# Optimization experiments

Measured on AMD Instinct MI355X. Metric: run time of the kernel, lower is better.

## Reference

```python
import jax, jax.numpy as jnp
import numpy as np

D, H, L, NB = 128, 8, 2, 32
NEIGHBOR_DIST = 50.0
OUT_H, PRED = 512, 60
N, A, T = 32, 50, 50
DH = D // H
FF = 4 * D


def setup_inputs():
    key = jax.random.key(0)
    ks = jax.random.split(key, 20)
    g = lambda k, s, sc=0.02: jax.random.normal(k, s, jnp.float32) * sc
    return {
        "x": jax.random.normal(ks[0], (N, A, T, 5), jnp.float32) * 10.0,
        "invalid_entries": jax.random.randint(ks[1], (N, A, T), 0, 2).astype(bool),
        "emb_W": g(ks[2], (5, D)), "emb_b": jnp.zeros((D,), jnp.float32),
        "dist_emb": g(ks[3], (NB, H)),
        "ln_g": jnp.ones((L, 3, D), jnp.float32), "ln_b": jnp.zeros((L, 3, D), jnp.float32),
        "Wq": g(ks[4], (L, 2, D, D)), "Wk": g(ks[5], (L, 2, D, D)),
        "Wv": g(ks[6], (L, 2, D, D)), "Wo": g(ks[7], (L, 2, D, D)),
        "ffn_W1": g(ks[8], (L, D, FF)), "ffn_b1": jnp.zeros((L, FF), jnp.float32),
        "ffn_W2": g(ks[9], (L, FF, D)), "ffn_b2": jnp.zeros((L, D), jnp.float32),
        "mlp_W1": g(ks[10], (D, OUT_H)), "mlp_b1": jnp.zeros((OUT_H,), jnp.float32),
        "mlp_W2": g(ks[11], (OUT_H, 2 * PRED)), "mlp_b2": jnp.zeros((2 * PRED,), jnp.float32),
    }


def _ln(h, g, b):
    mu = h.mean(-1, keepdims=True)
    var = ((h - mu) ** 2).mean(-1, keepdims=True)
    return (h - mu) / jnp.sqrt(var + 1e-5) * g + b


def _mha(h, Wq, Wk, Wv, Wo, mask, bias=None):
    # h: (B, S, D); mask: (B, S, S) bool, True = blocked; bias: (B, H, S, S)
    B, S, _ = h.shape
    q = (h @ Wq).reshape(B, S, H, DH)
    k = (h @ Wk).reshape(B, S, H, DH)
    v = (h @ Wv).reshape(B, S, H, DH)
    s = jnp.einsum('bqhd,bkhd->bhqk', q, k) / jnp.sqrt(jnp.float32(DH))
    if bias is not None:
        s = s + bias
    s = jnp.where(mask[:, None, :, :], jnp.float32(-1e9), s)
    a = jax.nn.softmax(s, axis=-1)
    o = jnp.einsum('bhqk,bkhd->bqhd', a, v).reshape(B, S, D)
    return o @ Wo


def _masks_and_bias(x, invalid_entries, dist_emb):
    # pos: (N*T, A, 2); masks are non-differentiable, stop grad through cdist
    pos = jax.lax.stop_gradient(jnp.swapaxes(x, 1, 2).reshape(N * T, A, 5)[:, :, :2])
    dist = jnp.sqrt(jnp.sum((pos[:, :, None, :] - pos[:, None, :, :]) ** 2, axis=-1))
    bin_size = NEIGHBOR_DIST / NB
    bucket = jnp.clip((dist / bin_size).astype(jnp.int32), 0, NB - 1)
    dist_bias = jnp.transpose(dist_emb[bucket], (0, 3, 1, 2))  # (N*T, H, A, A)

    inv_s = jnp.swapaxes(invalid_entries, 1, 2).reshape(N * T, A)
    ego_only = jnp.ones((A, A), bool).at[0, :].set(False)  # only ego row attends broadly
    social = (dist > NEIGHBOR_DIST) | inv_s[:, None, :] | ego_only[None]
    di_a = jnp.arange(min(50, A))
    social = social.at[:, di_a, di_a].set(False)  # vectorized form of the 50-iter loop

    inv_t = invalid_entries.reshape(N * A, T)
    temporal = jnp.triu(jnp.ones((T, T), bool), 1)[None] | inv_t[:, None, :]
    di_t = jnp.arange(min(50, T))
    temporal = temporal.at[:, di_t, di_t].set(False)
    return temporal, social, dist_bias


def _forward(x, invalid_entries, emb_W, emb_b, dist_emb, ln_g, ln_b,
             Wq, Wk, Wv, Wo, ffn_W1, ffn_b1, ffn_W2, ffn_b2,
             mlp_W1, mlp_b1, mlp_W2, mlp_b2):
    temporal_mask, social_mask, dist_bias = _masks_and_bias(x, invalid_entries, dist_emb)
    h = x @ emb_W + emb_b  # (N, A, T, D)
    for l in range(L):
        # temporal attention over T per agent
        ht = h.reshape(N * A, T, D)
        ht = ht + _mha(_ln(ht, ln_g[l, 0], ln_b[l, 0]),
                       Wq[l, 0], Wk[l, 0], Wv[l, 0], Wo[l, 0], temporal_mask)
        h = ht.reshape(N, A, T, D)
        # social attention over A per timestep, with bucketized distance bias
        hs = jnp.swapaxes(h, 1, 2).reshape(N * T, A, D)
        hs = hs + _mha(_ln(hs, ln_g[l, 1], ln_b[l, 1]),
                       Wq[l, 1], Wk[l, 1], Wv[l, 1], Wo[l, 1], social_mask, bias=dist_bias)
        h = jnp.swapaxes(hs.reshape(N, T, A, D), 1, 2)
        # FFN
        hn = _ln(h, ln_g[l, 2], ln_b[l, 2])
        h = h + (jnp.maximum(hn @ ffn_W1[l] + ffn_b1[l], 0.0) @ ffn_W2[l] + ffn_b2[l])
    e = h[:, 0]  # ego agent: (N, T, D)
    e = (e @ mlp_W1 + mlp_b1) @ mlp_W2 + mlp_b2  # two linears, no activation (as in source)
    return e.reshape(N, T, PRED, 2)


def reference(x, invalid_entries, emb_W, emb_b, dist_emb, ln_g, ln_b,
              Wq, Wk, Wv, Wo, ffn_W1, ffn_b1, ffn_W2, ffn_b2,
              mlp_W1, mlp_b1, mlp_W2, mlp_b2):
    return _forward(x, invalid_entries, emb_W, emb_b, dist_emb, ln_g, ln_b,
                    Wq, Wk, Wv, Wo, ffn_W1, ffn_b1, ffn_W2, ffn_b2,
                    mlp_W1, mlp_b1, mlp_W2, mlp_b2)
```

## Files before the change

### kernel.cpp

```cpp
#include <hip/hip_runtime.h>


#define DD 128
typedef __attribute__((ext_vector_type(8))) short bf16x8;
typedef __attribute__((ext_vector_type(4))) float f32x4;
#define MFMA16(a, b, c) __builtin_amdgcn_mfma_f32_16x16x32_bf16(a, b, c, 0, 0, 0)

__device__ __forceinline__ float bf2f(unsigned short u) {
  union { unsigned int i; float f; } x; x.i = ((unsigned int)u) << 16; return x.f;
}
__device__ __forceinline__ unsigned short f2bf(float f) {
  union { float f; unsigned int i; } x; x.f = f;
  return (unsigned short)((x.i + 0x7FFFu + ((x.i >> 16) & 1u)) >> 16);
}
__device__ __forceinline__ float wave_sum(float v) {
#pragma unroll
  for (int off = 32; off > 0; off >>= 1) v += __shfl_xor(v, off, 64);
  return v;
}
__device__ __forceinline__ float wave_max(float v) {
#pragma unroll
  for (int off = 32; off > 0; off >>= 1) v = fmaxf(v, __shfl_xor(v, off, 64));
  return v;
}
__device__ __forceinline__ bool load_inv(const void* p, int idx, int bytemode) {
  if (bytemode) return ((const unsigned char*)p)[idx] != 0;
  return ((const int*)p)[idx] != 0;
}

__global__ void detect_kernel(const void* __restrict__ inv, int* __restrict__ flag) {
  __shared__ int found;
  if (threadIdx.x == 0) found = 0;
  __syncthreads();
  const unsigned char* p = (const unsigned char*)inv;
  int loc = 0;
  for (int i = threadIdx.x; i < 16384; i += blockDim.x)
    if ((i & 3) != 0 && p[i] != 0) loc = 1;
  if (loc) atomicOr(&found, 1);
  __syncthreads();
  if (threadIdx.x == 0) *flag = found ? 1 : 0;
}

__global__ __launch_bounds__(256) void convert_weights(
    const float* __restrict__ Wq, const float* __restrict__ Wk,
    const float* __restrict__ Wv, const float* __restrict__ Wo,
    const float* __restrict__ W1, const float* __restrict__ W2,
    const float* __restrict__ W1m, const float* __restrict__ W2m,
    unsigned short* __restrict__ wqkv, unsigned short* __restrict__ wot,
    unsigned short* __restrict__ w1t, unsigned short* __restrict__ w2t,
    unsigned short* __restrict__ w1e, unsigned short* __restrict__ w2e) {
  __shared__ float tile[32][33];
  int b = blockIdx.x;
  int tx = threadIdx.x & 31, ty = threadIdx.x >> 5;
  const float* src; unsigned short* dst;
  int o0, i0, srcld, dstld, osub = 0, obound = 1 << 30;
  if (b < 192) {
    int m = b / 48, t2 = b % 48;
    o0 = (t2 / 4) * 32; i0 = (t2 % 4) * 32;
    int sel = o0 >> 7;
    src = (sel == 0 ? Wq : (sel == 1 ? Wk : Wv)) + m * 16384;
    osub = sel * 128; srcld = 128;
    dst = wqkv + m * 49152; dstld = 128;
  } else if (b < 256) {
    int m = (b - 192) / 16, t2 = (b - 192) % 16;
    o0 = (t2 / 4) * 32; i0 = (t2 % 4) * 32;
    src = Wo + m * 16384; srcld = 128;
    dst = wot + m * 16384; dstld = 128;
  } else if (b < 384) {
    int l = (b - 256) / 64, t2 = (b - 256) % 64;
    o0 = (t2 / 4) * 32; i0 = (t2 % 4) * 32;
    src = W1 + l * 65536; srcld = 512;
    dst = w1t + l * 65536; dstld = 128;
  } else if (b < 512) {
    int l = (b - 384) / 64, t2 = (b - 384) % 64;
    o0 = (t2 / 16) * 32; i0 = (t2 % 16) * 32;
    src = W2 + l * 65536; srcld = 128;
    dst = w2t + l * 65536; dstld = 512;
  } else if (b < 576) {
    int t2 = b - 512;
    o0 = (t2 / 4) * 32; i0 = (t2 % 4) * 32;
    src = W1m; srcld = 512;
    dst = w1e; dstld = 128;
  } else {
    int t2 = b - 576;
    o0 = (t2 / 16) * 32; i0 = (t2 % 16) * 32;
    src = W2m; srcld = 120; obound = 120;
    dst = w2e; dstld = 512;
  }
#pragma unroll
  for (int kk = 0; kk < 4; ++kk) {
    int i = i0 + ty + 8 * kk, o = o0 + tx;
    tile[ty + 8 * kk][tx] = (o < obound) ? src[i * srcld + (o - osub)] : 0.f;
  }
  __syncthreads();
#pragma unroll
  for (int kk = 0; kk < 4; ++kk) {
    int o = o0 + ty + 8 * kk, i = i0 + tx;
    dst[o * dstld + i] = f2bf(tile[tx][ty + 8 * kk]);
  }
}

__global__ __launch_bounds__(512, 4) void temporal_attn_kernel(
    const float* __restrict__ x, float* __restrict__ h,
    const void* __restrict__ inv, const int* __restrict__ flagp,
    const float* __restrict__ g, const float* __restrict__ bb,
    const float* __restrict__ embW, const float* __restrict__ embB,
    const unsigned short* __restrict__ wqkv,
    const unsigned short* __restrict__ wot, int first) {
  __shared__ __align__(16) unsigned short xbf[64][136];
  __shared__ __align__(16) unsigned short kbf[64][136];
  __shared__ __align__(16) unsigned short vT[128][72];
  __shared__ __align__(16) unsigned short pbuf[8][16][72];
  __shared__ float ssb[8][64];
  int seq = blockIdx.x;
  int tid = threadIdx.x, lane = tid & 63, wid = tid >> 6;
  unsigned long long invmask =
      __ballot((lane < 50) && load_inv(inv, seq * 50 + lane, *flagp));
  const f32x4 zf = (f32x4){0.f, 0.f, 0.f, 0.f};
  if (first) {
    for (int t = wid; t < 50; t += 8) {
      int tok = seq * 50 + t;
      float c0 = x[tok * 5], c1 = x[tok * 5 + 1], c2 = x[tok * 5 + 2];
      float c3 = x[tok * 5 + 3], c4 = x[tok * 5 + 4];
      float x0 = embB[lane] + c0 * embW[lane] + c1 * embW[128 + lane] +
                 c2 * embW[256 + lane] + c3 * embW[384 + lane] + c4 * embW[512 + lane];
      float x1 = embB[lane + 64] + c0 * embW[lane + 64] + c1 * embW[128 + lane + 64] +
                 c2 * embW[256 + lane + 64] + c3 * embW[384 + lane + 64] +
                 c4 * embW[512 + lane + 64];
      h[tok * DD + lane] = x0; h[tok * DD + lane + 64] = x1;
      float mu = wave_sum(x0 + x1) * (1.0f / 128.0f);
      float d0 = x0 - mu, d1 = x1 - mu;
      float var = wave_sum(d0 * d0 + d1 * d1) * (1.0f / 128.0f);
      float rstd = rsqrtf(var + 1e-5f);
      xbf[t][lane]      = f2bf(d0 * rstd * g[lane] + bb[lane]);
      xbf[t][lane + 64] = f2bf(d1 * rstd * g[lane + 64] + bb[lane + 64]);
    }
  } else {
    float v0[7], v1[7];
#pragma unroll
    for (int i = 0; i < 7; ++i) {
      int t = wid + 8 * i;
      if (t < 50) {
        v0[i] = h[(seq * 50 + t) * DD + lane];
        v1[i] = h[(seq * 50 + t) * DD + lane + 64];
      }
    }
#pragma unroll
    for (int i = 0; i < 7; ++i) {
      int t = wid + 8 * i;
      if (t < 50) {
        float mu = wave_sum(v0[i] + v1[i]) * (1.0f / 128.0f);
        float d0 = v0[i] - mu, d1 = v1[i] - mu;
        float var = wave_sum(d0 * d0 + d1 * d1) * (1.0f / 128.0f);
        float rstd = rsqrtf(var + 1e-5f);
        xbf[t][lane]      = f2bf(d0 * rstd * g[lane] + bb[lane]);
        xbf[t][lane + 64] = f2bf(d1 * rstd * g[lane + 64] + bb[lane + 64]);
      }
    }
  }
  for (int idx = tid; idx < 1904; idx += 512) {
    int r = idx / 136, cc = idx - r * 136;
    xbf[50 + r][cc] = 0;
    kbf[50 + r][cc] = 0;
  }
  for (int idx = tid; idx < 896; idx += 512) {
    int row = idx / 7, dwi = idx - row * 7;
    ((unsigned int*)&vT[row][50])[dwi] = 0u;
  }
  __syncthreads();
  int lrow = lane & 15, lk = (lane >> 4) * 8, lr4 = (lane >> 4) * 4;
  int colb = wid * 16 + lrow;
  {
    f32x4 ac[4];
#pragma unroll
    for (int mt = 0; mt < 4; ++mt) ac[mt] = zf;
    bf16x8 wk[4];
#pragma unroll
    for (int kt = 0; kt < 4; ++kt)
      wk[kt] = *(const bf16x8*)&wqkv[((8 + wid) * 16 + lrow) * 128 + kt * 32 + lk];
#pragma unroll
    for (int kt = 0; kt < 4; ++kt)
#pragma unroll
      for (int mt = 0; mt < 4; ++mt) {
        bf16x8 a = *(const bf16x8*)&xbf[mt * 16 + lrow][kt * 32 + lk];
        ac[mt] = MFMA16(a, wk[kt], ac[mt]);
      }
#pragma unroll
    for (int mt = 0; mt < 4; ++mt)
#pragma unroll
      for (int r = 0; r < 4; ++r) {
        int row = mt * 16 + lr4 + r;
        if (row < 50) kbf[row][colb] = f2bf(ac[mt][r]);
      }
  }
  {
    f32x4 ac[4];
#pragma unroll
    for (int mt = 0; mt < 4; ++mt) ac[mt] = zf;
    bf16x8 wv[4];
#pragma unroll
    for (int kt = 0; kt < 4; ++kt)
      wv[kt] = *(const bf16x8*)&wqkv[((16 + wid) * 16 + lrow) * 128 + kt * 32 + lk];
#pragma unroll
    for (int kt = 0; kt < 4; ++kt)
#pragma unroll
      for (int mt = 0; mt < 4; ++mt) {
        bf16x8 a = *(const bf16x8*)&xbf[mt * 16 + lrow][kt * 32 + lk];
        ac[mt] = MFMA16(a, wv[kt], ac[mt]);
      }
#pragma unroll
    for (int mt = 0; mt < 4; ++mt)
#pragma unroll
      for (int r = 0; r < 4; ++r) {
        int row = mt * 16 + lr4 + r;
        if (row < 50) vT[colb][row] = f2bf(ac[mt][r]);
      }
  }
  {
    f32x4 acQ[4];
#pragma unroll
    for (int mt = 0; mt < 4; ++mt) acQ[mt] = zf;
    bf16x8 wq[4];
#pragma unroll
    for (int kt = 0; kt < 4; ++kt)
      wq[kt] = *(const bf16x8*)&wqkv[(wid * 16 + lrow) * 128 + kt * 32 + lk];
#pragma unroll
    for (int kt = 0; kt < 4; ++kt)
#pragma unroll
      for (int mt = 0; mt < 4; ++mt) {
        bf16x8 a = *(const bf16x8*)&xbf[mt * 16 + lrow][kt * 32 + lk];
        acQ[mt] = MFMA16(a, wq[kt], acQ[mt]);
      }
    __syncthreads();
#pragma unroll
    for (int mt = 0; mt < 4; ++mt)
#pragma unroll
      for (int r = 0; r < 4; ++r) {
        int row = mt * 16 + lr4 + r;
        if (row < 50) xbf[row][colb] = f2bf(acQ[mt][r] * 0.25f);
      }
  }
  __syncthreads();
  {
    int hh = wid, c = lane & 15, gq = lane >> 4;
    const int hb = hh * 16;
    bf16x8 vfr0 = *(const bf16x8*)&vT[hb + c][gq * 8];
    bf16x8 vfr1 = *(const bf16x8*)&vT[hb + c][32 + gq * 8];
#pragma unroll
    for (int nt2 = 0; nt2 < 4; ++nt2) {
      bf16x8 qf = (bf16x8){0, 0, 0, 0, 0, 0, 0, 0};
      if (gq < 2) qf = *(const bf16x8*)&xbf[nt2 * 16 + c][hb + gq * 8];
      f32x4 Cs[4];
#pragma unroll
      for (int mt = 0; mt < 4; ++mt) {
        bf16x8 kf = (bf16x8){0, 0, 0, 0, 0, 0, 0, 0};
        if (gq < 2) kf = *(const bf16x8*)&kbf[mt * 16 + c][hb + gq * 8];
        Cs[mt] = MFMA16(kf, qf, zf);
      }
      int tq = nt2 * 16 + c;
      float ss = 0.f;
#pragma unroll
      for (int mt = 0; mt < 4; ++mt) {
        float pv[4];
#pragma unroll
        for (int r = 0; r < 4; ++r) {
          int tk = mt * 16 + gq * 4 + r;
          bool ok = (tk == tq) || ((tk < tq) && !((invmask >> tk) & 1ull));
          float p = ok ? __expf(Cs[mt][r]) : 0.f;
          ss += p;
          pv[r] = p;
        }
        unsigned int* dst = (unsigned int*)&pbuf[hh][c][mt * 16 + gq * 4];
        dst[0] = (unsigned)f2bf(pv[0]) | ((unsigned)f2bf(pv[1]) << 16);
        dst[1] = (unsigned)f2bf(pv[2]) | ((unsigned)f2bf(pv[3]) << 16);
      }
      ss += __shfl_xor(ss, 16, 64);
      ss += __shfl_xor(ss, 32, 64);
      if (gq == 0) ssb[hh][tq] = 1.f / ss;
      asm volatile("s_waitcnt lgkmcnt(0)" ::: "memory");
      __builtin_amdgcn_sched_barrier(0);
      bf16x8 pf0 = *(const bf16x8*)&pbuf[hh][c][gq * 8];
      bf16x8 pf1 = *(const bf16x8*)&pbuf[hh][c][32 + gq * 8];
      f32x4 acO = MFMA16(pf0, vfr0, zf);
      acO = MFMA16(pf1, vfr1, acO);
#pragma unroll
      for (int r = 0; r < 4; ++r) {
        int tqo = nt2 * 16 + gq * 4 + r;
        if (tqo < 50) {
          float rs = ssb[hh][tqo];
          xbf[tqo][hb + c] = f2bf(acO[r] * rs);
        }
      }
    }
  }
  __syncthreads();
  {
    f32x4 acc2[4];
#pragma unroll
    for (int mt = 0; mt < 4; ++mt) acc2[mt] = zf;
    bf16x8 wo4[4];
#pragma unroll
    for (int kt = 0; kt < 4; ++kt)
      wo4[kt] = *(const bf16x8*)&wot[(wid * 16 + lrow) * 128 + kt * 32 + lk];
#pragma unroll
    for (int kt = 0; kt < 4; ++kt)
#pragma unroll
      for (int mt = 0; mt < 4; ++mt) {
        bf16x8 a = *(const bf16x8*)&xbf[mt * 16 + lrow][kt * 32 + lk];
        acc2[mt] = MFMA16(a, wo4[kt], acc2[mt]);
      }
#pragma unroll
    for (int mt = 0; mt < 4; ++mt)
#pragma unroll
      for (int r = 0; r < 4; ++r) {
        int row = mt * 16 + lr4 + r;
        if (row < 50) h[(seq * 50 + row) * DD + colb] += acc2[mt][r];
      }
  }
}

__global__ __launch_bounds__(512, 6) void social_attn_kernel(
    const float* __restrict__ x, float* __restrict__ h,
    const void* __restrict__ inv, const int* __restrict__ flagp,
    const float* __restrict__ dist_emb,
    const float* __restrict__ g, const float* __restrict__ bb,
    const unsigned short* __restrict__ wqkv,
    const unsigned short* __restrict__ wot, int ego_only) {
  __shared__ __align__(16) unsigned short xbf[64][136];
  __shared__ __align__(16) unsigned short vsb[64][136];
  __shared__ float q0s[128];
  __shared__ float aw[8][52];
  int nt_ = blockIdx.x;
  int n = nt_ / 50, t = nt_ - n * 50;
  int tid = threadIdx.x, lane = tid & 63, wid = tid >> 6;
  const f32x4 zf = (f32x4){0.f, 0.f, 0.f, 0.f};
  {
    float v0[7], v1[7];
#pragma unroll
    for (int i = 0; i < 7; ++i) {
      int j = wid + 8 * i;
      if (j < 50) {
        int tok = (n * 50 + j) * 50 + t;
        v0[i] = h[tok * DD + lane];
        v1[i] = h[tok * DD + lane + 64];
      }
    }
#pragma unroll
    for (int i = 0; i < 7; ++i) {
      int j = wid + 8 * i;
      if (j < 50) {
        float mu = wave_sum(v0[i] + v1[i]) * (1.0f / 128.0f);
        float d0 = v0[i] - mu, d1 = v1[i] - mu;
        float var = wave_sum(d0 * d0 + d1 * d1) * (1.0f / 128.0f);
        float rstd = rsqrtf(var + 1e-5f);
        xbf[j][lane]      = f2bf(d0 * rstd * g[lane] + bb[lane]);
        xbf[j][lane + 64] = f2bf(d1 * rstd * g[lane + 64] + bb[lane + 64]);
      }
    }
  }
  __syncthreads();
  int lrow = lane & 15, lk = (lane >> 4) * 8, lr4 = (lane >> 4) * 4;
  int colb = wid * 16 + lrow;
  {
    f32x4 ac[4];
#pragma unroll
    for (int mt = 0; mt < 4; ++mt) ac[mt] = zf;
    bf16x8 wv[4];
#pragma unroll
    for (int kt = 0; kt < 4; ++kt)
      wv[kt] = *(const bf16x8*)&wqkv[((16 + wid) * 16 + lrow) * 128 + kt * 32 + lk];
#pragma unroll
    for (int kt = 0; kt < 4; ++kt)
#pragma unroll
      for (int mt = 0; mt < 4; ++mt) {
        bf16x8 a = *(const bf16x8*)&xbf[mt * 16 + lrow][kt * 32 + lk];
        ac[mt] = MFMA16(a, wv[kt], ac[mt]);
      }
#pragma unroll
    for (int mt = 0; mt < 4; ++mt)
#pragma unroll
      for (int r = 0; r < 4; ++r) {
        int row = mt * 16 + lr4 + r;
        if (row < 50) vsb[row][colb] = f2bf(ac[mt][r]);
      }
  }
  {
    f32x4 acq = zf;
    bf16x8 wq[4];
#pragma unroll
    for (int kt = 0; kt < 4; ++kt)
      wq[kt] = *(const bf16x8*)&wqkv[(wid * 16 + lrow) * 128 + kt * 32 + lk];
#pragma unroll
    for (int kt = 0; kt < 4; ++kt) {
      bf16x8 a0 = *(const bf16x8*)&xbf[lrow][kt * 32 + lk];
      acq = MFMA16(a0, wq[kt], acq);
    }
    if (lane < 16) q0s[wid * 16 + lane] = acq[0];
  }
  {
    f32x4 ac[4];
#pragma unroll
    for (int mt = 0; mt < 4; ++mt) ac[mt] = zf;
    bf16x8 wk[4];
#pragma unroll
    for (int kt = 0; kt < 4; ++kt)
      wk[kt] = *(const bf16x8*)&wqkv[((8 + wid) * 16 + lrow) * 128 + kt * 32 + lk];
#pragma unroll
    for (int kt = 0; kt < 4; ++kt)
#pragma unroll
      for (int mt = 0; mt < 4; ++mt) {
        bf16x8 a = *(const bf16x8*)&xbf[mt * 16 + lrow][kt * 32 + lk];
        ac[mt] = MFMA16(a, wk[kt], ac[mt]);
      }
    __syncthreads();
#pragma unroll
    for (int mt = 0; mt < 4; ++mt)
#pragma unroll
      for (int r = 0; r < 4; ++r) {
        int row = mt * 16 + lr4 + r;
        if (row < 50) xbf[row][colb] = f2bf(ac[mt][r]);
      }
  }
  __syncthreads();
  {
    int hh = wid, j = lane;
    float s = -1e30f;
    if (j < 50) {
      float x0 = x[(n * 2500 + t) * 5 + 0];
      float y0 = x[(n * 2500 + t) * 5 + 1];
      int tokj = (n * 50 + j) * 50 + t;
      float xj = x[tokj * 5 + 0], yj = x[tokj * 5 + 1];
      float dx = x0 - xj, dy = y0 - yj;
      float dist = sqrtf(dx * dx + dy * dy);
      int bucket = (int)(dist / 1.5625f);
      bucket = bucket < 0 ? 0 : (bucket > 31 ? 31 : bucket);
      bool mk = (j != 0) && ((dist > 50.0f) || load_inv(inv, tokj, *flagp));
      bf16x8 k0 = *(const bf16x8*)&xbf[j][hh * 16];
      bf16x8 k1 = *(const bf16x8*)&xbf[j][hh * 16 + 8];
      float acc2 = 0.f;
#pragma unroll
      for (int u = 0; u < 8; ++u)
        acc2 += q0s[hh * 16 + u] * bf2f((unsigned short)k0[u]) +
                q0s[hh * 16 + 8 + u] * bf2f((unsigned short)k1[u]);
      s = mk ? -1e9f : acc2 * 0.25f + dist_emb[bucket * 8 + hh];
    }
    float m = wave_max(s);
    float p = (j < 50) ? __expf(s - m) : 0.f;
    float sm = wave_sum(p);
    if (j < 50) aw[hh][j] = p / sm;
  }
  __syncthreads();
  float a0val = 0.f;
  if (tid < 128) {
    int hh2 = tid >> 4;
#pragma unroll 10
    for (int j = 0; j < 50; ++j) a0val += aw[hh2][j] * bf2f(vsb[j][tid]);
  }
  __syncthreads();
  if (tid < 128) vsb[0][tid] = f2bf(a0val);
  __syncthreads();
  if (!ego_only) {
    f32x4 acc2[4];
#pragma unroll
    for (int mt = 0; mt < 4; ++mt) acc2[mt] = zf;
    bf16x8 wo4[4];
#pragma unroll
    for (int kt = 0; kt < 4; ++kt)
      wo4[kt] = *(const bf16x8*)&wot[(wid * 16 + lrow) * 128 + kt * 32 + lk];
#pragma unroll
    for (int kt = 0; kt < 4; ++kt)
#pragma unroll
      for (int mt = 0; mt < 4; ++mt) {
        bf16x8 a = *(const bf16x8*)&vsb[mt * 16 + lrow][kt * 32 + lk];
        acc2[mt] = MFMA16(a, wo4[kt], acc2[mt]);
      }
#pragma unroll
    for (int mt = 0; mt < 4; ++mt)
#pragma unroll
      for (int r = 0; r < 4; ++r) {
        int row = mt * 16 + lr4 + r;
        if (row < 50)
          h[((n * 50 + row) * 50 + t) * DD + colb] += acc2[mt][r];
      }
  } else {
    f32x4 acc2 = zf;
    bf16x8 wo4[4];
#pragma unroll
    for (int kt = 0; kt < 4; ++kt)
      wo4[kt] = *(const bf16x8*)&wot[(wid * 16 + lrow) * 128 + kt * 32 + lk];
#pragma unroll
    for (int kt = 0; kt < 4; ++kt) {
      bf16x8 a = *(const bf16x8*)&vsb[lrow][kt * 32 + lk];
      acc2 = MFMA16(a, wo4[kt], acc2);
    }
    if ((lane >> 4) == 0)
      h[(n * 2500 + t) * DD + colb] += acc2[0];
  }
}

__global__ __launch_bounds__(512, 6) void ffn_kernel(
    float* __restrict__ h, const float* __restrict__ g, const float* __restrict__ bb,
    const unsigned short* __restrict__ w1t, const float* __restrict__ b1,
    const unsigned short* __restrict__ w2t, const float* __restrict__ b2) {
  __shared__ __align__(16) unsigned short xbf[32][136];
  __shared__ __align__(16) unsigned short hid[32][520];
  int base = blockIdx.x * 32;
  int tid = threadIdx.x, lane = tid & 63, wid = tid >> 6;
  {
    float v0[4], v1[4];
#pragma unroll
    for (int i = 0; i < 4; ++i) {
      int tok = base + wid + 8 * i;
      v0[i] = h[tok * DD + lane];
      v1[i] = h[tok * DD + lane + 64];
    }
#pragma unroll
    for (int i = 0; i < 4; ++i) {
      int r = wid + 8 * i;
      float mu = wave_sum(v0[i] + v1[i]) * (1.0f / 128.0f);
      float d0 = v0[i] - mu, d1 = v1[i] - mu;
      float var = wave_sum(d0 * d0 + d1 * d1) * (1.0f / 128.0f);
      float rstd = rsqrtf(var + 1e-5f);
      xbf[r][lane]      = f2bf(d0 * rstd * g[lane] + bb[lane]);
      xbf[r][lane + 64] = f2bf(d1 * rstd * g[lane + 64] + bb[lane + 64]);
    }
  }
  __syncthreads();
  int lrow = lane & 15, lk = (lane >> 4) * 8, lr4 = (lane >> 4) * 4;
  {
    f32x4 acc[2][4];
#pragma unroll
    for (int mt = 0; mt < 2; ++mt)
#pragma unroll
      for (int nt = 0; nt < 4; ++nt) acc[mt][nt] = (f32x4){0.f, 0.f, 0.f, 0.f};
    bf16x8 w[2][4];
#pragma unroll
    for (int nt = 0; nt < 4; ++nt)
      w[0][nt] = *(const bf16x8*)&w1t[(wid * 64 + nt * 16 + lrow) * 128 + lk];
#pragma unroll
    for (int kt = 0; kt < 4; ++kt) {
      if (kt < 3) {
#pragma unroll
        for (int nt = 0; nt < 4; ++nt)
          w[(kt + 1) & 1][nt] =
              *(const bf16x8*)&w1t[(wid * 64 + nt * 16 + lrow) * 128 + (kt + 1) * 32 + lk];
      }
      bf16x8 a0 = *(const bf16x8*)&xbf[lrow][kt * 32 + lk];
      bf16x8 a1 = *(const bf16x8*)&xbf[16 + lrow][kt * 32 + lk];
#pragma unroll
      for (int nt = 0; nt < 4; ++nt) {
        acc[0][nt] = MFMA16(a0, w[kt & 1][nt], acc[0][nt]);
        acc[1][nt] = MFMA16(a1, w[kt & 1][nt], acc[1][nt]);
      }
    }
#pragma unroll
    for (int nt = 0; nt < 4; ++nt) {
      int nn = wid * 64 + nt * 16 + lrow;
      float bias = b1[nn];
#pragma unroll
      for (int mt = 0; mt < 2; ++mt)
#pragma unroll
        for (int r = 0; r < 4; ++r)
          hid[mt * 16 + lr4 + r][nn] = f2bf(fmaxf(acc[mt][nt][r] + bias, 0.f));
    }
  }
  __syncthreads();
  {
    f32x4 acc2[2];
#pragma unroll
    for (int mt = 0; mt < 2; ++mt) acc2[mt] = (f32x4){0.f, 0.f, 0.f, 0.f};
    int nn = wid * 16 + lrow;
    bf16x8 w[2][4];
#pragma unroll
    for (int kk = 0; kk < 4; ++kk)
      w[0][kk] = *(const bf16x8*)&w2t[nn * 512 + kk * 32 + lk];
#pragma unroll
    for (int gph = 0; gph < 4; ++gph) {
      if (gph < 3) {
#pragma unroll
        for (int kk = 0; kk < 4; ++kk)
          w[(gph + 1) & 1][kk] =
              *(const bf16x8*)&w2t[nn * 512 + ((gph + 1) * 4 + kk) * 32 + lk];
      }
#pragma unroll
      for (int kk = 0; kk < 4; ++kk) {
        int kt = gph * 4 + kk;
        bf16x8 a0 = *(const bf16x8*)&hid[lrow][kt * 32 + lk];
        bf16x8 a1 = *(const bf16x8*)&hid[16 + lrow][kt * 32 + lk];
        acc2[0] = MFMA16(a0, w[gph & 1][kk], acc2[0]);
        acc2[1] = MFMA16(a1, w[gph & 1][kk], acc2[1]);
      }
    }
    float bias = b2[nn];
#pragma unroll
    for (int mt = 0; mt < 2; ++mt)
#pragma unroll
      for (int r = 0; r < 4; ++r)
        h[(base + mt * 16 + lr4 + r) * DD + nn] += acc2[mt][r] + bias;
  }
}

__global__ __launch_bounds__(256) void ffn_ego_kernel(
    const float* __restrict__ h,
    const float* __restrict__ g2, const float* __restrict__ bb2,
    const unsigned short* __restrict__ w1t, const float* __restrict__ b1,
    const unsigned short* __restrict__ w2t, const float* __restrict__ b2,
    const unsigned short* __restrict__ w1e, const float* __restrict__ b1m,
    const unsigned short* __restrict__ w2e, const float* __restrict__ b2m,
    float* __restrict__ out) {
  __shared__ float hx[16][132];
  __shared__ __align__(16) unsigned short xln[16][136];
  __shared__ __align__(16) unsigned short hid[16][520];
  int base = blockIdx.x * 16;
  int tid = threadIdx.x, lane = tid & 63, wid = tid >> 6;
  const f32x4 zf = (f32x4){0.f, 0.f, 0.f, 0.f};
  for (int idx = tid; idx < 2048; idx += 256) {
    int r = idx >> 7, d = idx & 127;
    int nt = base + r, n = nt / 50, t = nt - n * 50;
    hx[r][d] = h[(n * 2500 + t) * DD + d];
  }
  __syncthreads();
  for (int r = wid; r < 16; r += 4) {
    float x0 = hx[r][lane], x1 = hx[r][lane + 64];
    float mu = wave_sum(x0 + x1) * (1.0f / 128.0f);
    float d0 = x0 - mu, d1 = x1 - mu;
    float var = wave_sum(d0 * d0 + d1 * d1) * (1.0f / 128.0f);
    float rstd = rsqrtf(var + 1e-5f);
    xln[r][lane]      = f2bf(d0 * rstd * g2[lane] + bb2[lane]);
    xln[r][lane + 64] = f2bf(d1 * rstd * g2[lane + 64] + bb2[lane + 64]);
  }
  __syncthreads();
  int lrow = lane & 15, lk = (lane >> 4) * 8, lr4 = (lane >> 4) * 4;
  {
    f32x4 acc[8];
#pragma unroll
    for (int nt = 0; nt < 8; ++nt) acc[nt] = zf;
#pragma unroll
    for (int kt = 0; kt < 4; ++kt) {
      bf16x8 a = *(const bf16x8*)&xln[lrow][kt * 32 + lk];
#pragma unroll
      for (int nt = 0; nt < 8; ++nt) {
        int nn = wid * 128 + nt * 16 + lrow;
        bf16x8 bfr = *(const bf16x8*)&w1t[nn * 128 + kt * 32 + lk];
        acc[nt] = MFMA16(a, bfr, acc[nt]);
      }
    }
#pragma unroll
    for (int nt = 0; nt < 8; ++nt) {
      int nn = wid * 128 + nt * 16 + lrow;
      float bias = b1[nn];
#pragma unroll
      for (int r = 0; r < 4; ++r)
        hid[lr4 + r][nn] = f2bf(fmaxf(acc[nt][r] + bias, 0.f));
    }
  }
  __syncthreads();
  {
    f32x4 acc2[2];
#pragma unroll
    for (int nt = 0; nt < 2; ++nt) acc2[nt] = zf;
#pragma unroll
    for (int kt = 0; kt < 16; ++kt) {
      bf16x8 a = *(const bf16x8*)&hid[lrow][kt * 32 + lk];
#pragma unroll
      for (int nt = 0; nt < 2; ++nt) {
        int nn = wid * 32 + nt * 16 + lrow;
        bf16x8 bfr = *(const bf16x8*)&w2t[nn * 512 + kt * 32 + lk];
        acc2[nt] = MFMA16(a, bfr, acc2[nt]);
      }
    }
#pragma unroll
    for (int nt = 0; nt < 2; ++nt) {
      int nn = wid * 32 + nt * 16 + lrow;
      float bias = b2[nn];
#pragma unroll
      for (int r = 0; r < 4; ++r)
        xln[lr4 + r][nn] = f2bf(hx[lr4 + r][nn] + acc2[nt][r] + bias);
    }
  }
  __syncthreads();
  {
    f32x4 acc[8];
#pragma unroll
    for (int nt = 0; nt < 8; ++nt) acc[nt] = zf;
#pragma unroll
    for (int kt = 0; kt < 4; ++kt) {
      bf16x8 a = *(const bf16x8*)&xln[lrow][kt * 32 + lk];
#pragma unroll
      for (int nt = 0; nt < 8; ++nt) {
        int nn = wid * 128 + nt * 16 + lrow;
        bf16x8 bfr = *(const bf16x8*)&w1e[nn * 128 + kt * 32 + lk];
        acc[nt] = MFMA16(a, bfr, acc[nt]);
      }
    }
    __syncthreads();
#pragma unroll
    for (int nt = 0; nt < 8; ++nt) {
      int nn = wid * 128 + nt * 16 + lrow;
      float bias = b1m[nn];
#pragma unroll
      for (int r = 0; r < 4; ++r)
        hid[lr4 + r][nn] = f2bf(acc[nt][r] + bias);
    }
  }
  __syncthreads();
  {
    f32x4 acc2[2];
#pragma unroll
    for (int nt = 0; nt < 2; ++nt) acc2[nt] = zf;
#pragma unroll
    for (int kt = 0; kt < 16; ++kt) {
      bf16x8 a = *(const bf16x8*)&hid[lrow][kt * 32 + lk];
#pragma unroll
      for (int nt = 0; nt < 2; ++nt) {
        int nn = wid * 32 + nt * 16 + lrow;
        bf16x8 bfr = *(const bf16x8*)&w2e[nn * 512 + kt * 32 + lk];
        acc2[nt] = MFMA16(a, bfr, acc2[nt]);
      }
    }
#pragma unroll
    for (int nt = 0; nt < 2; ++nt) {
      int nn = wid * 32 + nt * 16 + lrow;
      if (nn < 120) {
        float bias = b2m[nn];
#pragma unroll
        for (int r = 0; r < 4; ++r)
          out[(base + lr4 + r) * 120 + nn] = acc2[nt][r] + bias;
      }
    }
  }
}

extern "C" void kernel_launch(void* const* d_in, const int* in_sizes, int n_in,
                              void* d_out, int out_size, void* d_ws, size_t ws_size,
                              hipStream_t stream) {
  const float* x        = (const float*)d_in[0];
  const void*  inv      = d_in[1];
  const float* emb_W    = (const float*)d_in[2];
  const float* emb_b    = (const float*)d_in[3];
  const float* dist_emb = (const float*)d_in[4];
  const float* ln_g     = (const float*)d_in[5];
  const float* ln_b     = (const float*)d_in[6];
  const float* Wq       = (const float*)d_in[7];
  const float* Wk       = (const float*)d_in[8];
  const float* Wv       = (const float*)d_in[9];
  const float* Wo       = (const float*)d_in[10];
  const float* ffn_W1   = (const float*)d_in[11];
  const float* ffn_b1   = (const float*)d_in[12];
  const float* ffn_W2   = (const float*)d_in[13];
  const float* ffn_b2   = (const float*)d_in[14];
  const float* mlp_W1   = (const float*)d_in[15];
  const float* mlp_b1   = (const float*)d_in[16];
  const float* mlp_W2   = (const float*)d_in[17];
  const float* mlp_b2   = (const float*)d_in[18];
  float* out = (float*)d_out;

  float* ws = (float*)d_ws;
  float* h  = ws;
  unsigned short* wbf = (unsigned short*)(ws + 10240000);
  unsigned short* wqkv = wbf;
  unsigned short* wot  = wbf + 196608;
  unsigned short* w1t  = wbf + 262144;
  unsigned short* w2t  = wbf + 393216;
  unsigned short* w1e  = wbf + 524288;
  unsigned short* w2e  = wbf + 589824;
  int* flag = (int*)(ws + 10600000);

  detect_kernel<<<dim3(1), dim3(256), 0, stream>>>(inv, flag);
  convert_weights<<<dim3(640), dim3(256), 0, stream>>>(
      Wq, Wk, Wv, Wo, ffn_W1, ffn_W2, mlp_W1, mlp_W2,
      wqkv, wot, w1t, w2t, w1e, w2e);
  temporal_attn_kernel<<<dim3(1600), dim3(512), 0, stream>>>(
      x, h, inv, flag, ln_g + 0 * DD, ln_b + 0 * DD, emb_W, emb_b,
      wqkv + 0 * 49152, wot + 0 * 16384, 1);
  social_attn_kernel<<<dim3(1600), dim3(512), 0, stream>>>(
      x, h, inv, flag, dist_emb, ln_g + 1 * DD, ln_b + 1 * DD,
      wqkv + 1 * 49152, wot + 1 * 16384, 0);
  ffn_kernel<<<dim3(2500), dim3(512), 0, stream>>>(
      h, ln_g + 2 * DD, ln_b + 2 * DD, w1t, ffn_b1, w2t, ffn_b2);
  temporal_attn_kernel<<<dim3(1600), dim3(512), 0, stream>>>(
      x, h, inv, flag, ln_g + 3 * DD, ln_b + 3 * DD, emb_W, emb_b,
      wqkv + 2 * 49152, wot + 2 * 16384, 0);
  social_attn_kernel<<<dim3(1600), dim3(512), 0, stream>>>(
      x, h, inv, flag, dist_emb, ln_g + 4 * DD, ln_b + 4 * DD,
      wqkv + 3 * 49152, wot + 3 * 16384, 1);
  ffn_ego_kernel<<<dim3(100), dim3(256), 0, stream>>>(
      h, ln_g + 5 * DD, ln_b + 5 * DD,
      w1t + 65536, ffn_b1 + 512, w2t + 65536, ffn_b2 + 128,
      w1e, mlp_b1, w2e, mlp_b2, out);
}
```

Baseline: 369.2 us.

## Process 64 tokens per FFN block to reuse second-layer weight fragments

```diff
diff --git a/kernel.cpp b/kernel.cpp
--- a/kernel.cpp
+++ b/kernel.cpp
@@ -498,102 +498,87 @@
   }
 }
 
-__global__ __launch_bounds__(512, 6) void ffn_kernel(
+__global__ __launch_bounds__(512, 4) void ffn_kernel(
     float* __restrict__ h, const float* __restrict__ g, const float* __restrict__ bb,
     const unsigned short* __restrict__ w1t, const float* __restrict__ b1,
     const unsigned short* __restrict__ w2t, const float* __restrict__ b2) {
   __shared__ __align__(16) unsigned short xbf[32][136];
-  __shared__ __align__(16) unsigned short hid[32][520];
-  int base = blockIdx.x * 32;
+  __shared__ __align__(16) unsigned short hid[64][520];
+  int base = blockIdx.x * 64;
   int tid = threadIdx.x, lane = tid & 63, wid = tid >> 6;
-  {
-    float v0[4], v1[4];
-#pragma unroll
-    for (int i = 0; i < 4; ++i) {
-      int tok = base + wid + 8 * i;
-      v0[i] = h[tok * DD + lane];
-      v1[i] = h[tok * DD + lane + 64];
-    }
-#pragma unroll
-    for (int i = 0; i < 4; ++i) {
-      int r = wid + 8 * i;
-      float mu = wave_sum(v0[i] + v1[i]) * (1.0f / 128.0f);
-      float d0 = v0[i] - mu, d1 = v1[i] - mu;
-      float var = wave_sum(d0 * d0 + d1 * d1) * (1.0f / 128.0f);
-      float rstd = rsqrtf(var + 1e-5f);
-      xbf[r][lane]      = f2bf(d0 * rstd * g[lane] + bb[lane]);
-      xbf[r][lane + 64] = f2bf(d1 * rstd * g[lane + 64] + bb[lane + 64]);
-    }
-  }
-  __syncthreads();
   int lrow = lane & 15, lk = (lane >> 4) * 8, lr4 = (lane >> 4) * 4;
-  {
-    f32x4 acc[2][4];
-#pragma unroll
-    for (int mt = 0; mt < 2; ++mt)
-#pragma unroll
-      for (int nt = 0; nt < 4; ++nt) acc[mt][nt] = (f32x4){0.f, 0.f, 0.f, 0.f};
-    bf16x8 w[2][4];
-#pragma unroll
-    for (int nt = 0; nt < 4; ++nt)
-      w[0][nt] = *(const bf16x8*)&w1t[(wid * 64 + nt * 16 + lrow) * 128 + lk];
-#pragma unroll
-    for (int kt = 0; kt < 4; ++kt) {
-      if (kt < 3) {
-#pragma unroll
-        for (int nt = 0; nt < 4; ++nt)
-          w[(kt + 1) & 1][nt] =
-              *(const bf16x8*)&w1t[(wid * 64 + nt * 16 + lrow) * 128 + (kt + 1) * 32 + lk];
-      }
-      bf16x8 a0 = *(const bf16x8*)&xbf[lrow][kt * 32 + lk];
-      bf16x8 a1 = *(const bf16x8*)&xbf[16 + lrow][kt * 32 + lk];
+#pragma unroll 1
+  for (int s = 0; s < 2; ++s) {
+    int tb = base + s * 32;
+    {
+      float v0[4], v1[4];
+#pragma unroll
+      for (int i = 0; i < 4; ++i) {
+        int tok = tb + wid + 8 * i;
+        v0[i] = h[tok * DD + lane];
+        v1[i] = h[tok * DD + lane + 64];
+      }
+#pragma unroll
+      for (int i = 0; i < 4; ++i) {
+        int r = wid + 8 * i;
+        float mu = wave_sum(v0[i] + v1[i]) * (1.0f / 128.0f);
+        float d0 = v0[i] - mu, d1 = v1[i] - mu;
+        float var = wave_sum(d0 * d0 + d1 * d1) * (1.0f / 128.0f);
+        float rstd = rsqrtf(var + 1e-5f);
+        xbf[r][lane]      = f2bf(d0 * rstd * g[lane] + bb[lane]);
+        xbf[r][lane + 64] = f2bf(d1 * rstd * g[lane + 64] + bb[lane + 64]);
+      }
+    }
+    __syncthreads();
+    {
+      f32x4 acc[2][4];
+#pragma unroll
+      for (int mt = 0; mt < 2; ++mt)
+#pragma unroll
+        for (int nt = 0; nt < 4; ++nt) acc[mt][nt] = (f32x4){0.f, 0.f, 0.f, 0.f};
+#pragma unroll
+      for (int kt = 0; kt < 4; ++kt) {
+        bf16x8 a0 = *(const bf16x8*)&xbf[lrow][kt * 32 + lk];
+        bf16x8 a1 = *(const bf16x8*)&xbf[16 + lrow][kt * 32 + lk];
+#pragma unroll
+        for (int nt = 0; nt < 4; ++nt) {
+          int nn = wid * 64 + nt * 16 + lrow;
+          bf16x8 bfr = *(const bf16x8*)&w1t[nn * 128 + kt * 32 + lk];
+          acc[0][nt] = MFMA16(a0, bfr, acc[0][nt]);
+          acc[1][nt] = MFMA16(a1, bfr, acc[1][nt]);
+        }
+      }
 #pragma unroll
       for (int nt = 0; nt < 4; ++nt) {
-        acc[0][nt] = MFMA16(a0, w[kt & 1][nt], acc[0][nt]);
-        acc[1][nt] = MFMA16(a1, w[kt & 1][nt], acc[1][nt]);
-      }
-    }
-#pragma unroll
-    for (int nt = 0; nt < 4; ++nt) {
-      int nn = wid * 64 + nt * 16 + lrow;
-      float bias = b1[nn];
-#pragma unroll
-      for (int mt = 0; mt < 2; ++mt)
-#pragma unroll
-        for (int r = 0; r < 4; ++r)
-          hid[mt * 16 + lr4 + r][nn] = f2bf(fmaxf(acc[mt][nt][r] + bias, 0.f));
-    }
-  }
-  __syncthreads();
-  {
-    f32x4 acc2[2];
-#pragma unroll
-    for (int mt = 0; mt < 2; ++mt) acc2[mt] = (f32x4){0.f, 0.f, 0.f, 0.f};
+        int nn = wid * 64 + nt * 16 + lrow;
+        float bias = b1[nn];
+#pragma unroll
+        for (int mt = 0; mt < 2; ++mt)
+#pragma unroll
+          for (int r = 0; r < 4; ++r)
+            hid[s * 32 + mt * 16 + lr4 + r][nn] =
+                f2bf(fmaxf(acc[mt][nt][r] + bias, 0.f));
+      }
+    }
+    __syncthreads();
+  }
+  {
+    f32x4 acc2[4];
+#pragma unroll
+    for (int mt = 0; mt < 4; ++mt) acc2[mt] = (f32x4){0.f, 0.f, 0.f, 0.f};
     int nn = wid * 16 + lrow;
-    bf16x8 w[2][4];
-#pragma unroll
-    for (int kk = 0; kk < 4; ++kk)
-      w[0][kk] = *(const bf16x8*)&w2t[nn * 512 + kk * 32 + lk];
-#pragma unroll
-    for (int gph = 0; gph < 4; ++gph) {
-      if (gph < 3) {
-#pragma unroll
-        for (int kk = 0; kk < 4; ++kk)
-          w[(gph + 1) & 1][kk] =
-              *(const bf16x8*)&w2t[nn * 512 + ((gph + 1) * 4 + kk) * 32 + lk];
-      }
-#pragma unroll
-      for (int kk = 0; kk < 4; ++kk) {
-        int kt = gph * 4 + kk;
-        bf16x8 a0 = *(const bf16x8*)&hid[lrow][kt * 32 + lk];
-        bf16x8 a1 = *(const bf16x8*)&hid[16 + lrow][kt * 32 + lk];
-        acc2[0] = MFMA16(a0, w[gph & 1][kk], acc2[0]);
-        acc2[1] = MFMA16(a1, w[gph & 1][kk], acc2[1]);
+#pragma unroll
+    for (int kt = 0; kt < 16; ++kt) {
+      bf16x8 bfr = *(const bf16x8*)&w2t[nn * 512 + kt * 32 + lk];
+#pragma unroll
+      for (int mt = 0; mt < 4; ++mt) {
+        bf16x8 a = *(const bf16x8*)&hid[mt * 16 + lrow][kt * 32 + lk];
+        acc2[mt] = MFMA16(a, bfr, acc2[mt]);
       }
     }
     float bias = b2[nn];
 #pragma unroll
-    for (int mt = 0; mt < 2; ++mt)
+    for (int mt = 0; mt < 4; ++mt)
 #pragma unroll
       for (int r = 0; r < 4; ++r)
         h[(base + mt * 16 + lr4 + r) * DD + nn] += acc2[mt][r] + bias;
@@ -776,7 +761,7 @@
   social_attn_kernel<<<dim3(1600), dim3(512), 0, stream>>>(
       x, h, inv, flag, dist_emb, ln_g + 1 * DD, ln_b + 1 * DD,
       wqkv + 1 * 49152, wot + 1 * 16384, 0);
-  ffn_kernel<<<dim3(2500), dim3(512), 0, stream>>>(
+  ffn_kernel<<<dim3(1250), dim3(512), 0, stream>>>(
       h, ln_g + 2 * DD, ln_b + 2 * DD, w1t, ffn_b1, w2t, ffn_b2);
   temporal_attn_kernel<<<dim3(1600), dim3(512), 0, stream>>>(
       x, h, inv, flag, ln_g + 3 * DD, ln_b + 3 * DD, emb_W, emb_b,
```

Result: faster. 338.7 us (-8.3%).
